# Performance work log

Hardware: AMD Instinct MI355X
Metric: run time of the kernel (lower is better)

Reference implementation:

```python
import jax, jax.numpy as jnp
import numpy as np

B, N, D = 4, 2048, 2048
HEADS, KV_HEADS = 16, 4
DH = D // HEADS            # 128 per-head dim
KV_RATIO = HEADS // KV_HEADS
MAX_LEN, MAX_BSZ = 2048, 4
EPS = 1.1920929e-07        # torch.finfo(float32).eps (RMSNorm default eps=None)


def _rot_tables(n, d, base=10000.0):
    thetas = base ** (-jnp.arange(0, d, 2, dtype=jnp.float32) / d)   # [d/2]
    ang = jnp.arange(n, dtype=jnp.float32)[:, None] * thetas[None, :]
    cos = jnp.repeat(jnp.cos(ang), 2, axis=-1)   # [n, d] interleaved pairs
    sin = jnp.repeat(jnp.sin(ang), 2, axis=-1)
    return cos, sin


def _rotate_half_inverted(x):
    x1 = x[..., ::2]
    x2 = x[..., 1::2]
    return jnp.stack([-x2, x1], axis=-1).reshape(x.shape)


def _apply_rotation(x, end, start=0):
    cos, sin = _rot_tables(MAX_LEN, DH)
    return x * cos[start:end] + _rotate_half_inverted(x) * sin[start:end]


def setup_inputs() -> dict:
    key = jax.random.key(0)
    ks = jax.random.split(key, 4)
    s = 0.02
    return {
        "x": jax.random.normal(ks[0], (B, N, D), jnp.float32),
        "norm_w": jnp.ones((D,), jnp.float32),
        "qw": jax.random.normal(ks[1], (HEADS * DH, D), jnp.float32) * s,
        "qb": jnp.zeros((HEADS * DH,), jnp.float32),
        "kvw": jax.random.normal(ks[2], (2 * DH * KV_HEADS, D), jnp.float32) * s,
        "kvb": jnp.zeros((2 * DH * KV_HEADS,), jnp.float32),
        "wow": jax.random.normal(ks[3], (D, HEADS * DH), jnp.float32) * s,
        "wob": jnp.zeros((D,), jnp.float32),
        "kv_cache": jnp.zeros((MAX_BSZ, MAX_LEN, 2 * DH * KV_HEADS), jnp.float32),
        "pos": 0,
    }


def reference(x, norm_w, qw, qb, kvw, kvb, wow, wob, kv_cache, pos):
    b, n, d = x.shape
    t = pos + n  # total cached length
    # RMSNorm
    xn = x * jax.lax.rsqrt(jnp.mean(x * x, axis=-1, keepdims=True) + EPS) * norm_w
    # Q projection -> [b, heads, n, dh]
    q = (xn @ qw.T + qb).reshape(b, n, HEADS, DH).transpose(0, 2, 1, 3)
    # KV projection + cache write/read
    kv = xn @ kvw.T + kvb                                  # [b, n, 2*dh*kv_heads]
    cache = jax.lax.dynamic_update_slice(kv_cache, kv, (0, pos, 0))
    kvf = cache[:b, :t].reshape(b, t, KV_HEADS, 2 * DH).transpose(0, 2, 1, 3)
    kvf = jnp.repeat(kvf, KV_RATIO, axis=1)                # GQA expand -> [b, heads, t, 2dh]
    k, v = kvf[..., :DH], kvf[..., DH:]
    # RoPE (interleaved-pair variant)
    q = _apply_rotation(q, t, pos)
    k = _apply_rotation(k, t, 0)
    # Attention (decoder causal)
    attn = jnp.einsum("bhqd,bhkd->bhqk", q, k) / jnp.sqrt(jnp.float32(DH))
    if n > 1:
        mask = jnp.triu(jnp.ones((n, t), bool), k=1 + pos)
        attn = jnp.where(mask, -jnp.inf, attn)
    attn = jax.nn.softmax(attn, axis=-1)
    o = jnp.einsum("bhqk,bhkd->bhqd", attn, v).transpose(0, 2, 1, 3).reshape(b, n, HEADS * DH)
    return o @ wow.T + wob
```

## Files before the change

kernel.cpp:

```cpp
#include <hip/hip_runtime.h>
#include <hip/hip_bf16.h>

typedef unsigned short u16;
typedef unsigned int u32;
typedef __attribute__((ext_vector_type(4))) float f32x4;
typedef __attribute__((ext_vector_type(8))) short s16x8;

#define B_ 4
#define N_ 2048
#define D_ 2048
#define HEADS_ 16
#define KVH_ 4
#define DH_ 128
#define KVD_ 1024
#define M_ 8192
#define SCALE_ 0.08838834764831845f
#define QSCALE2_ 0.12753257518622628f

__device__ __forceinline__ u16 f2bf(float f) {
  u32 u = __builtin_bit_cast(u32, f);
  return (u16)((u + 0x7FFFu + ((u >> 16) & 1u)) >> 16);
}

__device__ __forceinline__ float fexp2(float x) {
#if __has_builtin(__builtin_amdgcn_exp2f)
  return __builtin_amdgcn_exp2f(x);
#else
  return exp2f(x);
#endif
}

__device__ __forceinline__ void gload_lds16(const void* g, void* l) {
  __builtin_amdgcn_global_load_lds(
      (const __attribute__((address_space(1))) u32*)g,
      (__attribute__((address_space(3))) u32*)l, 16, 0, 0);
}

__global__ __launch_bounds__(256)
void rope_tab_k(float* __restrict__ cost, float* __restrict__ sint)
{
  const int idx = blockIdx.x * 256 + threadIdx.x;
  const int p = idx >> 6, i = idx & 63;
  const float theta = expf(-(float)i * 0.015625f * 9.210340371976184f);
  float s, c;
  sincosf((float)p * theta, &s, &c);
  cost[idx] = c;
  sint[idx] = s;
}

__global__ __launch_bounds__(256)
void cvt_bf16_k(const float* __restrict__ s, u16* __restrict__ d, int n)
{
  const int i = (blockIdx.x * 256 + threadIdx.x) * 8;
  if (i >= n) return;
  const f32x4 a = *(const f32x4*)(s + i);
  const f32x4 b = *(const f32x4*)(s + i + 4);
  s16x8 o;
  #pragma unroll
  for (int j = 0; j < 4; ++j) { o[j] = (short)f2bf(a[j]); o[4 + j] = (short)f2bf(b[j]); }
  *(s16x8*)(d + i) = o;
}

__global__ __launch_bounds__(256)
void rmsnorm_k(const float* __restrict__ x, const float* __restrict__ w, u16* __restrict__ xn)
{
  const int row = blockIdx.x, t = threadIdx.x;
  const float* xr = x + (size_t)row * D_;
  const f32x4 a = *(const f32x4*)(xr + t * 8);
  const f32x4 b = *(const f32x4*)(xr + t * 8 + 4);
  float ss = a[0]*a[0] + a[1]*a[1] + a[2]*a[2] + a[3]*a[3]
           + b[0]*b[0] + b[1]*b[1] + b[2]*b[2] + b[3]*b[3];
  #pragma unroll
  for (int off = 32; off >= 1; off >>= 1) ss += __shfl_xor(ss, off);
  __shared__ float wss[4];
  if ((t & 63) == 0) wss[t >> 6] = ss;
  __syncthreads();
  const float tot = wss[0] + wss[1] + wss[2] + wss[3];
  const float rs = rsqrtf(tot * (1.0f / D_) + 1.1920929e-07f);
  s16x8 o;
  #pragma unroll
  for (int j = 0; j < 4; ++j) {
    o[j]     = (short)f2bf(a[j] * rs * w[t * 8 + j]);
    o[4 + j] = (short)f2bf(b[j] * rs * w[t * 8 + 4 + j]);
  }
  *(s16x8*)(xn + (size_t)row * D_ + t * 8) = o;
}

template<int EPI>
__global__ __launch_bounds__(256)
void gemm_bt(const u16* __restrict__ A, const u16* __restrict__ Bw,
             void* __restrict__ Cv, void* __restrict__ Cv2,
             const float* __restrict__ bias, const float* __restrict__ bias2,
             int N, int K,
             const float* __restrict__ cos_t, const float* __restrict__ sin_t)
{
  __shared__ u16 As[128 * 32];
  __shared__ u16 Bs[128 * 32];
  const int t = threadIdx.x;
  const int w = t >> 6, lane = t & 63;
  const int g = lane >> 4, lr = lane & 15;
  const int row0 = blockIdx.x * 128, col0 = blockIdx.y * 128;
  const int wr = (w >> 1) * 64, wc = (w & 1) * 64;

  f32x4 acc[4][4] = {};

  const u16* gA = A + (size_t)(row0 + w * 16 + (lane >> 2)) * K + (lane & 3) * 8;
  const u16* gB = Bw + (size_t)(col0 + w * 16 + (lane >> 2)) * K + (lane & 3) * 8;
  u16* lA = As + (w * 16) * 32;
  u16* lB = Bs + (w * 16) * 32;

  for (int kt = 0; kt < K; kt += 32) {
    #pragma unroll
    for (int r = 0; r < 2; ++r) {
      gload_lds16(gA + (size_t)(r * 64) * K + kt, lA + r * 64 * 32);
      gload_lds16(gB + (size_t)(r * 64) * K + kt, lB + r * 64 * 32);
    }
    __syncthreads();
    s16x8 af[4], bf[4];
    #pragma unroll
    for (int i = 0; i < 4; ++i) {
      af[i] = *(const s16x8*)(As + (wr + i * 16 + lr) * 32 + g * 8);
      bf[i] = *(const s16x8*)(Bs + (wc + i * 16 + lr) * 32 + g * 8);
    }
    #pragma unroll
    for (int mi = 0; mi < 4; ++mi)
      #pragma unroll
      for (int ni = 0; ni < 4; ++ni)
        acc[mi][ni] = __builtin_amdgcn_mfma_f32_16x16x32_bf16(af[mi], bf[ni], acc[mi][ni], 0, 0, 0);
    __syncthreads();
  }

  #pragma unroll
  for (int mi = 0; mi < 4; ++mi) {
    #pragma unroll
    for (int ni = 0; ni < 4; ++ni) {
      const int cc = col0 + wc + ni * 16 + lr;
      const float bv = (cc >= 2048) ? bias2[cc - 2048] : bias[cc];
      #pragma unroll
      for (int j = 0; j < 4; ++j) {
        const int rr = row0 + wr + mi * 16 + g * 4 + j;
        float v = acc[mi][ni][j] + bv;
        const int pos = rr & (N_ - 1);
        const float pv = __shfl_xor(v, 1);
        if (cc < 2048) {
          const int d = cc & (DH_ - 1);
          const float c = cos_t[pos * 64 + (d >> 1)];
          const float s = sin_t[pos * 64 + (d >> 1)];
          const float o = (cc & 1) ? fmaf(v, c, pv * s) : fmaf(v, c, -pv * s);
          ((u16*)Cv)[(size_t)rr * 2048 + cc] = f2bf(o);
        } else {
          const int ccc = cc - 2048;
          const int dm = ccc & 255;
          float o = v;
          if (dm < DH_) {
            const float c = cos_t[pos * 64 + (dm >> 1)];
            const float s = sin_t[pos * 64 + (dm >> 1)];
            o = (dm & 1) ? fmaf(v, c, pv * s) : fmaf(v, c, -pv * s);
          }
          ((u16*)Cv2)[(size_t)rr * 1024 + ccc] = f2bf(o);
        }
      }
    }
  }
}

__global__ __launch_bounds__(512, 1)
void gemm256(const u16* __restrict__ A, const u16* __restrict__ Bw,
             float* __restrict__ Cv, const float* __restrict__ bias)
{
  __shared__ __align__(16) u16 As[2][16384];
  __shared__ __align__(16) u16 Bs[2][16384];
  const int t = threadIdx.x, w = t >> 6, l = t & 63;
  const int g = l >> 4, lr = l & 15;
  const int wm = w >> 2, wn = w & 3;
  const int row0 = blockIdx.y * 256, col0 = blockIdx.x * 256;
  const int NT = 2048 / 64;

  const int sr = l >> 3;
  const int sc = ((l & 7) * 8) ^ (sr << 3);
  const u16* gA = A  + (size_t)(row0 + w * 8 + sr) * 2048 + sc;
  const u16* gB = Bw + (size_t)(col0 + w * 8 + sr) * 2048 + sc;

  f32x4 acc[8][4] = {};

  auto stage_tile = [&](int kt2, int pb) {
    #pragma unroll
    for (int q = 0; q < 4; ++q) {
      gload_lds16(gA + (size_t)(q * 64) * 2048 + kt2 * 64, &As[pb][(q * 8 + w) * 512]);
      gload_lds16(gB + (size_t)(q * 64) * 2048 + kt2 * 64, &Bs[pb][(q * 8 + w) * 512]);
    }
  };
  auto ldf = [&](const u16* base, int row, int ks) -> s16x8 {
    const int ba = row * 128 + ((ks * 64 + g * 16) ^ ((lr & 7) << 4));
    return *(const s16x8*)((const char*)base + ba);
  };

  stage_tile(0, 0);

  for (int kt = 0; kt < NT; ++kt) {
    const int p = kt & 1;
    if (kt + 1 < NT) {
      stage_tile(kt + 1, p ^ 1);
      asm volatile("s_waitcnt vmcnt(8)" ::: "memory");
    } else {
      asm volatile("s_waitcnt vmcnt(0)" ::: "memory");
    }
    __builtin_amdgcn_s_barrier();

    const u16* Ap = &As[p][0];
    const u16* Bp = &Bs[p][0];
    s16x8 af[4][2], bf[4][2];
    #pragma unroll
    for (int nf = 0; nf < 4; ++nf)
      #pragma unroll
      for (int ks = 0; ks < 2; ++ks) bf[nf][ks] = ldf(Bp, wn * 64 + nf * 16 + lr, ks);
    #pragma unroll
    for (int mf = 0; mf < 4; ++mf)
      #pragma unroll
      for (int ks = 0; ks < 2; ++ks) af[mf][ks] = ldf(Ap, wm * 128 + mf * 16 + lr, ks);
    __builtin_amdgcn_s_setprio(1);
    #pragma unroll
    for (int mf = 0; mf < 4; ++mf)
      #pragma unroll
      for (int nf = 0; nf < 4; ++nf)
        #pragma unroll
        for (int ks = 0; ks < 2; ++ks)
          acc[mf][nf] = __builtin_amdgcn_mfma_f32_16x16x32_bf16(af[mf][ks], bf[nf][ks], acc[mf][nf], 0, 0, 0);
    __builtin_amdgcn_s_setprio(0);
    #pragma unroll
    for (int mf = 0; mf < 4; ++mf)
      #pragma unroll
      for (int ks = 0; ks < 2; ++ks) af[mf][ks] = ldf(Ap, wm * 128 + (4 + mf) * 16 + lr, ks);
    __builtin_amdgcn_s_setprio(1);
    #pragma unroll
    for (int mf = 0; mf < 4; ++mf)
      #pragma unroll
      for (int nf = 0; nf < 4; ++nf)
        #pragma unroll
        for (int ks = 0; ks < 2; ++ks)
          acc[4 + mf][nf] = __builtin_amdgcn_mfma_f32_16x16x32_bf16(af[mf][ks], bf[nf][ks], acc[4 + mf][nf], 0, 0, 0);
    __builtin_amdgcn_s_setprio(0);
    __builtin_amdgcn_sched_barrier(0);
    __builtin_amdgcn_s_barrier();
  }

  #pragma unroll
  for (int mf = 0; mf < 8; ++mf) {
    #pragma unroll
    for (int nf = 0; nf < 4; ++nf) {
      const int cc = col0 + wn * 64 + nf * 16 + lr;
      const float bv = bias[cc];
      #pragma unroll
      for (int j = 0; j < 4; ++j) {
        const int rr = row0 + wm * 128 + mf * 16 + g * 4 + j;
        Cv[(size_t)rr * 2048 + cc] = acc[mf][nf][j] + bv;
      }
    }
  }
}

__global__ __launch_bounds__(256)
void vtrans_k(const u16* __restrict__ kvb, u16* __restrict__ vt)
{
  __shared__ u16 tile[64][65];
  const int z = blockIdx.z, b = z >> 2, kh = z & 3;
  const int p0 = blockIdx.x * 64, d0 = blockIdx.y * 64;
  const int t = threadIdx.x;
  #pragma unroll
  for (int r = 0; r < 2; ++r) {
    const int pl = r * 32 + (t >> 3), dl = (t & 7) * 8;
    const s16x8 v = *(const s16x8*)(kvb + (size_t)(b * N_ + p0 + pl) * KVD_ + kh * 256 + 128 + d0 + dl);
    #pragma unroll
    for (int jj = 0; jj < 8; ++jj) tile[pl][dl + jj] = (u16)v[jj];
  }
  __syncthreads();
  #pragma unroll
  for (int r = 0; r < 2; ++r) {
    const int dl = r * 32 + (t >> 3), pl = (t & 7) * 8;
    s16x8 o;
    #pragma unroll
    for (int jj = 0; jj < 8; ++jj) o[jj] = (short)tile[pl + jj][dl];
    *(s16x8*)(vt + ((size_t)(z * DH_ + d0 + dl)) * N_ + p0 + pl) = o;
  }
}

__global__ __launch_bounds__(512, 2)
void attn_k(const u16* __restrict__ q, const u16* __restrict__ kvb,
            const u16* __restrict__ vt, u16* __restrict__ out)
{
  const int fi = blockIdx.x, h = blockIdx.y, b = blockIdx.z;
  const int kh = h >> 2;
  const int t = threadIdx.x, w = t >> 6, lane = t & 63;
  const int g = lane >> 4, lr = lane & 15;

  __shared__ __align__(16) u16 Ks[2][64 * 128];
  __shared__ __align__(16) u16 Vs[2][128 * 64];
  __shared__ __align__(16) u16 Ps[8][16 * 64];

  const int kc = 2 * w;
  const int kr0 = kc * 4 + (lane >> 4);
  const int ksw0 = (lane & 15) ^ (kr0 & 7);
  const int kr1 = kr0 + 4;
  const int ksw1 = (lane & 15) ^ (kr1 & 7);
  const int vd0 = kc * 8 + (lane >> 3);
  const int vsw0 = (lane & 7) ^ (vd0 & 7);
  const int vd1 = vd0 + 8;
  const int vsw1 = (lane & 7) ^ (vd1 & 7);

  const u16* kbase = kvb + (size_t)b * (N_ * KVD_) + kh * 256;
  const u16* vbase = vt + (size_t)((b * KVH_ + kh) * DH_) * N_;

  int cur = 0;

  auto issue = [&](int kt, int buf) {
    gload_lds16(kbase + (size_t)(kt * 64 + kr0) * KVD_ + ksw0 * 8, &Ks[buf][kc * 512]);
    gload_lds16(kbase + (size_t)(kt * 64 + kr1) * KVD_ + ksw1 * 8, &Ks[buf][(kc + 1) * 512]);
    gload_lds16(vbase + (size_t)vd0 * N_ + kt * 64 + vsw0 * 8, &Vs[buf][kc * 512]);
    gload_lds16(vbase + (size_t)vd1 * N_ + kt * 64 + vsw1 * 8, &Vs[buf][(kc + 1) * 512]);
  };

  auto run_qtile = [&](int qi, int nkt, bool chain) {
    const int qrow0 = qi * 128 + w * 16;
    const int td = qrow0 >> 6;
    s16x8 qf[4];
    {
      const u16* qp = q + (size_t)(b * N_ + qrow0 + lr) * D_ + h * DH_;
      #pragma unroll
      for (int ks = 0; ks < 4; ++ks) qf[ks] = *(const s16x8*)(qp + ks * 32 + g * 8);
    }
    f32x4 o_acc[8] = {};
    float m_j[4], l_j[4];
    #pragma unroll
    for (int j = 0; j < 4; ++j) { m_j[j] = -1e30f; l_j[j] = 0.0f; }

    for (int kt = 0; kt < nkt; ++kt) {
      __syncthreads();
      if (kt + 1 < nkt)      issue(kt + 1, cur ^ 1);
      else if (chain)        issue(0, cur ^ 1);

      if (kt <= td) {
        const u16* Kc = &Ks[cur][0];
        const u16* Vc = &Vs[cur][0];

        f32x4 sf[4] = {};
        __builtin_amdgcn_s_setprio(1);
        #pragma unroll
        for (int ks = 0; ks < 4; ++ks) {
          #pragma unroll
          for (int kvf = 0; kvf < 4; ++kvf) {
            const int kvr = kvf * 16 + lr;
            const int ba = (kvr * 256 + ks * 64 + g * 16) ^ ((kvr & 7) << 4);
            const s16x8 kf = *(const s16x8*)((const char*)Kc + ba);
            sf[kvf] = __builtin_amdgcn_mfma_f32_16x16x32_bf16(qf[ks], kf, sf[kvf], 0, 0, 0);
          }
        }
        __builtin_amdgcn_s_setprio(0);

        const bool need_mask = (kt == td);
        float pmax[4];
        #pragma unroll
        for (int j = 0; j < 4; ++j) {
          float mx = -1e30f;
          #pragma unroll
          for (int kvf = 0; kvf < 4; ++kvf) {
            float sv = sf[kvf][j] * QSCALE2_;
            if (need_mask) {
              const int kj = kt * 64 + kvf * 16 + lr;
              const int qi_row = qrow0 + g * 4 + j;
              if (kj > qi_row) sv = -1e30f;
            }
            sf[kvf][j] = sv;
            mx = fmaxf(mx, sv);
          }
          mx = fmaxf(mx, __shfl_xor(mx, 1));
          mx = fmaxf(mx, __shfl_xor(mx, 2));
          mx = fmaxf(mx, __shfl_xor(mx, 4));
          mx = fmaxf(mx, __shfl_xor(mx, 8));
          pmax[j] = mx;
        }

        const float needv = fmaxf(fmaxf(pmax[0] - m_j[0], pmax[1] - m_j[1]),
                                  fmaxf(pmax[2] - m_j[2], pmax[3] - m_j[3]));
        if (__any(needv > 8.0f)) {
          #pragma unroll
          for (int j = 0; j < 4; ++j) {
            const float mn = fmaxf(m_j[j], pmax[j]);
            const float pf = fexp2(m_j[j] - mn);
            m_j[j] = mn;
            l_j[j] *= pf;
            #pragma unroll
            for (int df = 0; df < 8; ++df) o_acc[df][j] *= pf;
          }
        }

        #pragma unroll
        for (int j = 0; j < 4; ++j) {
          float lacc = 0.0f;
          #pragma unroll
          for (int kvf = 0; kvf < 4; ++kvf) {
            const float p = fexp2(sf[kvf][j] - m_j[j]);
            lacc += p;
            const int rq = g * 4 + j, ck = kvf * 16 + lr;
            const int ba = (rq * 128 + ck * 2) ^ ((rq & 7) << 4);
            *(u16*)((char*)&Ps[w][0] + ba) = (u16)(__builtin_bit_cast(u32, p) >> 16);
          }
          l_j[j] += lacc;
        }

        __builtin_amdgcn_s_setprio(1);
        #pragma unroll
        for (int kk = 0; kk < 2; ++kk) {
          const int bap = (lr * 128 + kk * 64 + g * 16) ^ ((lr & 7) << 4);
          const s16x8 pf = *(const s16x8*)((const char*)&Ps[w][0] + bap);
          #pragma unroll
          for (int df = 0; df < 8; ++df) {
            const int dd = df * 16 + lr;
            const int bav = (dd * 128 + kk * 64 + g * 16) ^ ((dd & 7) << 4);
            const s16x8 vf = *(const s16x8*)((const char*)Vc + bav);
            o_acc[df] = __builtin_amdgcn_mfma_f32_16x16x32_bf16(pf, vf, o_acc[df], 0, 0, 0);
          }
        }
        __builtin_amdgcn_s_setprio(0);
      }
      cur ^= 1;
    }

    float inv_l[4];
    #pragma unroll
    for (int j = 0; j < 4; ++j) {
      float s4 = l_j[j];
      s4 += __shfl_xor(s4, 1);
      s4 += __shfl_xor(s4, 2);
      s4 += __shfl_xor(s4, 4);
      s4 += __shfl_xor(s4, 8);
      inv_l[j] = 1.0f / s4;
    }
    u16* op = out + (size_t)(b * N_ + qrow0) * D_ + h * DH_;
    #pragma unroll
    for (int df = 0; df < 8; ++df)
      #pragma unroll
      for (int j = 0; j < 4; ++j)
        op[(size_t)(g * 4 + j) * D_ + df * 16 + lr] = f2bf(o_acc[df][j] * inv_l[j]);
  };

  const int qlo = fi, qhi = 15 - fi;
  issue(0, 0);
  run_qtile(qlo, 2 * qlo + 2, true);
  run_qtile(qhi, 2 * qhi + 2, false);
}

extern "C" void kernel_launch(void* const* d_in, const int* in_sizes, int n_in,
                              void* d_out, int out_size, void* d_ws, size_t ws_size,
                              hipStream_t stream) {
  const float* x      = (const float*)d_in[0];
  const float* normw  = (const float*)d_in[1];
  const float* qw     = (const float*)d_in[2];
  const float* qbias  = (const float*)d_in[3];
  const float* kvw    = (const float*)d_in[4];
  const float* kvbias = (const float*)d_in[5];
  const float* wow    = (const float*)d_in[6];
  const float* wob    = (const float*)d_in[7];
  float* out = (float*)d_out;

  char* ws = (char*)d_ws;
  u16* xn    = (u16*)(ws + 0);
  u16* dq    = (u16*)(ws + 33554432);
  u16* dkv   = (u16*)(ws + 67108864);
  u16* dvt   = (u16*)(ws + 83886080);
  u16* wqkv  = (u16*)(ws + 92274688);
  u16* wowb  = (u16*)(ws + 104857600);
  float* cost = (float*)(ws + 113246208);
  float* sint = (float*)(ws + 113770496);

  rope_tab_k<<<512, 256, 0, stream>>>(cost, sint);
  cvt_bf16_k<<<2048, 256, 0, stream>>>(qw, wqkv, 2048 * 2048);
  cvt_bf16_k<<<1024, 256, 0, stream>>>(kvw, wqkv + 2048 * 2048, 1024 * 2048);
  cvt_bf16_k<<<2048, 256, 0, stream>>>(wow, wowb, 2048 * 2048);
  rmsnorm_k<<<8192, 256, 0, stream>>>(x, normw, xn);
  gemm_bt<4><<<dim3(64, 24), 256, 0, stream>>>(xn, wqkv, (void*)dq, (void*)dkv,
                                               qbias, kvbias, 3072, 2048, cost, sint);
  vtrans_k<<<dim3(32, 2, 16), 256, 0, stream>>>(dkv, dvt);
  attn_k<<<dim3(8, 16, 4), 512, 0, stream>>>(dq, dkv, dvt, xn);
  gemm256<<<dim3(8, 32), 512, 0, stream>>>(xn, wowb, out, wob);
}
```

Baseline: 431.0 us.

## Rewrite QKV GEMM with 256x128 tiles, double-buffered swizzled LDS pipeline

Replaces the simple 128x128 single-buffered QKV projection GEMM with a 512-thread 256x128 tile kernel. It uses double-buffered LDS with XOR-swizzled layout, a 64-wide K step, and prefetches the next tile while computing the current one using explicit vmcnt waits. It also raises MFMA priority around the compute block. This aims to hide global-load latency, cut LDS bank conflicts and per-iteration barriers. In exchange it uses more LDS per block and allows only one block per CU.

New measurement: 437.2 us. No clear change (+1.4%).

```diff
diff --git a/kernel.cpp b/kernel.cpp
--- a/kernel.cpp
+++ b/kernel.cpp
@@ -14,7 +14,6 @@
 #define DH_ 128
 #define KVD_ 1024
 #define M_ 8192
-#define SCALE_ 0.08838834764831845f
 #define QSCALE2_ 0.12753257518622628f
 
 __device__ __forceinline__ u16 f2bf(float f) {
@@ -86,60 +85,86 @@
   *(s16x8*)(xn + (size_t)row * D_ + t * 8) = o;
 }
 
-template<int EPI>
-__global__ __launch_bounds__(256)
-void gemm_bt(const u16* __restrict__ A, const u16* __restrict__ Bw,
-             void* __restrict__ Cv, void* __restrict__ Cv2,
-             const float* __restrict__ bias, const float* __restrict__ bias2,
-             int N, int K,
+__global__ __launch_bounds__(512, 1)
+void gemmqkv(const u16* __restrict__ A, const u16* __restrict__ Bw,
+             u16* __restrict__ dq, u16* __restrict__ dkv,
+             const float* __restrict__ qbias, const float* __restrict__ kvbias,
              const float* __restrict__ cos_t, const float* __restrict__ sin_t)
 {
-  __shared__ u16 As[128 * 32];
-  __shared__ u16 Bs[128 * 32];
-  const int t = threadIdx.x;
-  const int w = t >> 6, lane = t & 63;
-  const int g = lane >> 4, lr = lane & 15;
-  const int row0 = blockIdx.x * 128, col0 = blockIdx.y * 128;
-  const int wr = (w >> 1) * 64, wc = (w & 1) * 64;
+  __shared__ __align__(16) u16 As[2][16384];
+  __shared__ __align__(16) u16 Bs[2][8192];
+  const int t = threadIdx.x, w = t >> 6, l = t & 63;
+  const int g = l >> 4, lr = l & 15;
+  const int wm = w >> 1, wn = w & 1;
+  const int row0 = blockIdx.y * 256, col0 = blockIdx.x * 128;
+  const int NT = 32;
+
+  const int sr = l >> 3;
+  const int sc = ((l & 7) * 8) ^ (sr << 3);
+  const u16* gA = A  + (size_t)(row0 + w * 8 + sr) * 2048 + sc;
+  const u16* gB = Bw + (size_t)(col0 + w * 8 + sr) * 2048 + sc;
 
   f32x4 acc[4][4] = {};
 
-  const u16* gA = A + (size_t)(row0 + w * 16 + (lane >> 2)) * K + (lane & 3) * 8;
-  const u16* gB = Bw + (size_t)(col0 + w * 16 + (lane >> 2)) * K + (lane & 3) * 8;
-  u16* lA = As + (w * 16) * 32;
-  u16* lB = Bs + (w * 16) * 32;
-
-  for (int kt = 0; kt < K; kt += 32) {
-    #pragma unroll
-    for (int r = 0; r < 2; ++r) {
-      gload_lds16(gA + (size_t)(r * 64) * K + kt, lA + r * 64 * 32);
-      gload_lds16(gB + (size_t)(r * 64) * K + kt, lB + r * 64 * 32);
-    }
-    __syncthreads();
-    s16x8 af[4], bf[4];
-    #pragma unroll
-    for (int i = 0; i < 4; ++i) {
-      af[i] = *(const s16x8*)(As + (wr + i * 16 + lr) * 32 + g * 8);
-      bf[i] = *(const s16x8*)(Bs + (wc + i * 16 + lr) * 32 + g * 8);
-    }
-    #pragma unroll
-    for (int mi = 0; mi < 4; ++mi)
-      #pragma unroll
-      for (int ni = 0; ni < 4; ++ni)
-        acc[mi][ni] = __builtin_amdgcn_mfma_f32_16x16x32_bf16(af[mi], bf[ni], acc[mi][ni], 0, 0, 0);
-    __syncthreads();
-  }
-
-  #pragma unroll
-  for (int mi = 0; mi < 4; ++mi) {
-    #pragma unroll
-    for (int ni = 0; ni < 4; ++ni) {
-      const int cc = col0 + wc + ni * 16 + lr;
-      const float bv = (cc >= 2048) ? bias2[cc - 2048] : bias[cc];
+  auto stage_tile = [&](int kt2, int pb) {
+    #pragma unroll
+    for (int q = 0; q < 4; ++q)
+      gload_lds16(gA + (size_t)(q * 64) * 2048 + kt2 * 64, &As[pb][(q * 8 + w) * 512]);
+    #pragma unroll
+    for (int q = 0; q < 2; ++q)
+      gload_lds16(gB + (size_t)(q * 64) * 2048 + kt2 * 64, &Bs[pb][(q * 8 + w) * 512]);
+  };
+  auto ldf = [&](const u16* base, int row, int ks) -> s16x8 {
+    const int ba = row * 128 + ((ks * 64 + g * 16) ^ ((lr & 7) << 4));
+    return *(const s16x8*)((const char*)base + ba);
+  };
+
+  stage_tile(0, 0);
+
+  for (int kt = 0; kt < NT; ++kt) {
+    const int p = kt & 1;
+    if (kt + 1 < NT) {
+      stage_tile(kt + 1, p ^ 1);
+      asm volatile("s_waitcnt vmcnt(6)" ::: "memory");
+    } else {
+      asm volatile("s_waitcnt vmcnt(0)" ::: "memory");
+    }
+    __builtin_amdgcn_s_barrier();
+
+    const u16* Ap = &As[p][0];
+    const u16* Bp = &Bs[p][0];
+    s16x8 af[4][2], bf[4][2];
+    #pragma unroll
+    for (int nf = 0; nf < 4; ++nf)
+      #pragma unroll
+      for (int ks = 0; ks < 2; ++ks) bf[nf][ks] = ldf(Bp, wn * 64 + nf * 16 + lr, ks);
+    #pragma unroll
+    for (int mf = 0; mf < 4; ++mf)
+      #pragma unroll
+      for (int ks = 0; ks < 2; ++ks) af[mf][ks] = ldf(Ap, wm * 64 + mf * 16 + lr, ks);
+    __builtin_amdgcn_s_setprio(1);
+    #pragma unroll
+    for (int mf = 0; mf < 4; ++mf)
+      #pragma unroll
+      for (int nf = 0; nf < 4; ++nf)
+        #pragma unroll
+        for (int ks = 0; ks < 2; ++ks)
+          acc[mf][nf] = __builtin_amdgcn_mfma_f32_16x16x32_bf16(af[mf][ks], bf[nf][ks], acc[mf][nf], 0, 0, 0);
+    __builtin_amdgcn_s_setprio(0);
+    __builtin_amdgcn_sched_barrier(0);
+    __builtin_amdgcn_s_barrier();
+  }
+
+  #pragma unroll
+  for (int mf = 0; mf < 4; ++mf) {
+    #pragma unroll
+    for (int nf = 0; nf < 4; ++nf) {
+      const int cc = col0 + wn * 64 + nf * 16 + lr;
+      const float bv = (cc >= 2048) ? kvbias[cc - 2048] : qbias[cc];
       #pragma unroll
       for (int j = 0; j < 4; ++j) {
-        const int rr = row0 + wr + mi * 16 + g * 4 + j;
-        float v = acc[mi][ni][j] + bv;
+        const int rr = row0 + wm * 64 + mf * 16 + g * 4 + j;
+        float v = acc[mf][nf][j] + bv;
         const int pos = rr & (N_ - 1);
         const float pv = __shfl_xor(v, 1);
         if (cc < 2048) {
@@ -147,7 +172,7 @@
           const float c = cos_t[pos * 64 + (d >> 1)];
           const float s = sin_t[pos * 64 + (d >> 1)];
           const float o = (cc & 1) ? fmaf(v, c, pv * s) : fmaf(v, c, -pv * s);
-          ((u16*)Cv)[(size_t)rr * 2048 + cc] = f2bf(o);
+          dq[(size_t)rr * 2048 + cc] = f2bf(o);
         } else {
           const int ccc = cc - 2048;
           const int dm = ccc & 255;
@@ -157,7 +182,7 @@
             const float s = sin_t[pos * 64 + (dm >> 1)];
             o = (dm & 1) ? fmaf(v, c, pv * s) : fmaf(v, c, -pv * s);
           }
-          ((u16*)Cv2)[(size_t)rr * 1024 + ccc] = f2bf(o);
+          dkv[(size_t)rr * 1024 + ccc] = f2bf(o);
         }
       }
     }
@@ -477,8 +502,7 @@
   cvt_bf16_k<<<1024, 256, 0, stream>>>(kvw, wqkv + 2048 * 2048, 1024 * 2048);
   cvt_bf16_k<<<2048, 256, 0, stream>>>(wow, wowb, 2048 * 2048);
   rmsnorm_k<<<8192, 256, 0, stream>>>(x, normw, xn);
-  gemm_bt<4><<<dim3(64, 24), 256, 0, stream>>>(xn, wqkv, (void*)dq, (void*)dkv,
-                                               qbias, kvbias, 3072, 2048, cost, sint);
+  gemmqkv<<<dim3(24, 32), 512, 0, stream>>>(xn, wqkv, dq, dkv, qbias, kvbias, cost, sint);
   vtrans_k<<<dim3(32, 2, 16), 256, 0, stream>>>(dkv, dvt);
   attn_k<<<dim3(8, 16, 4), 512, 0, stream>>>(dq, dkv, dvt, xn);
   gemm256<<<dim3(8, 32), 512, 0, stream>>>(xn, wowb, out, wob);
```
